# Performance work log

Measured on AMD Instinct MI355X. Metric: run time of the kernel, lower is better.

The kernel has to match this reference:

```python
import jax, jax.numpy as jnp
import numpy as np

P = 3; C = 64; IMG = 48; G = IMG // P
D = C * P * P          # 576 embedding dim == flatten dim
NH = 12; HD = D // NH  # 48 head dim
HID = 4 * D            # 2304
NL = 4; S = G * G      # 256 patches
NQ = 6
QN, QP = -8.0, 7.0     # 4-bit signed LSQ range
EPS = 1e-5


def lsq(w):
    # LSQ fake-quant of weights, step size from LSQ init formula, STE rounding
    alpha = 2.0 * jnp.mean(jnp.abs(w)) / jnp.sqrt(QP)
    q = jnp.clip(w / alpha, QN, QP)
    q = q + jax.lax.stop_gradient(jnp.round(q) - q)
    return q * alpha


def qlinear(x, w, b=None):
    y = x @ lsq(w).T
    return y if b is None else y + b


def ln(x, g, b):
    m = jnp.mean(x, -1, keepdims=True)
    v = jnp.var(x, -1, keepdims=True)
    return (x - m) / jnp.sqrt(v + EPS) * g + b


def mha(q, k, v, in_w, out_w):
    # q,k,v: [S,B,D]; in_w: [3D,D]; out_w: [D,D]; no biases
    Wq, Wk, Wv = jnp.split(lsq(in_w), 3, axis=0)
    def heads(t, W):
        return (t @ W.T).reshape(t.shape[0], t.shape[1], NH, HD)
    qh = heads(q, Wq) * (1.0 / jnp.sqrt(HD))
    kh = heads(k, Wk)
    vh = heads(v, Wv)
    att = jax.nn.softmax(jnp.einsum('qbhd,kbhd->bhqk', qh, kh), axis=-1)
    o = jnp.einsum('bhqk,kbhd->qbhd', att, vh).reshape(q.shape[0], q.shape[1], D)
    return o @ lsq(out_w).T


def _forward(x, lin_enc_w, lin_enc_b, pos_emb, query_embed_w,
             enc_in_w, enc_out_w, enc_l1_w, enc_l1_b, enc_l2_w, enc_l2_b,
             enc_ln1_g, enc_ln1_b, enc_ln2_g, enc_ln2_b,
             dec_sa_in_w, dec_sa_out_w, dec_ca_in_w, dec_ca_out_w,
             dec_l1_w, dec_l1_b, dec_l2_w, dec_l2_b,
             dec_ln1_g, dec_ln1_b, dec_ln2_g, dec_ln2_b, dec_ln3_g, dec_ln3_b,
             head1_w, head1_b, head2_w, head2_b, query_idx):
    B = x.shape[0]
    # unfold -> [S,B,flat], channel-major patch flattening like F.unfold
    t = x.reshape(B, C, G, P, G, P).transpose(0, 1, 3, 5, 2, 4)
    t = t.reshape(B, C * P * P, G * G).transpose(2, 0, 1)  # [S,B,D]
    t = qlinear(t, lin_enc_w, lin_enc_b) + t
    qe = query_embed_w[query_idx].reshape(S, 1, D)   # query_pos, broadcasts over B
    pos = pos_emb[:, None, :]                        # [S,1,D]
    h = t + pos
    for l in range(NL):  # encoder (pre-norm)
        h2 = ln(h, enc_ln1_g[l], enc_ln1_b[l])
        h = h + mha(h2, h2, h2, enc_in_w[l], enc_out_w[l])
        h2 = ln(h, enc_ln2_g[l], enc_ln2_b[l])
        h = h + qlinear(jax.nn.relu(qlinear(h2, enc_l1_w[l], enc_l1_b[l])), enc_l2_w[l], enc_l2_b[l])
    mem = h
    o = mem
    for l in range(NL):  # decoder, memory = encoder output
        o2 = ln(o, dec_ln1_g[l], dec_ln1_b[l])
        qk = o2 + qe
        o = o + mha(qk, qk, o2, dec_sa_in_w[l], dec_sa_out_w[l])
        o2 = ln(o, dec_ln2_g[l], dec_ln2_b[l])
        o = o + mha(o2 + qe, mem, mem, dec_ca_in_w[l], dec_ca_out_w[l])
        o2 = ln(o, dec_ln3_g[l], dec_ln3_b[l])
        o = o + qlinear(jax.nn.relu(qlinear(o2, dec_l1_w[l], dec_l1_b[l])), dec_l2_w[l], dec_l2_b[l])
    # mlp_head with residual
    o = o + qlinear(jax.nn.relu(qlinear(o, head1_w, head1_b)), head2_w, head2_b)
    # fold back: [S,B,D] -> [B,C,IMG,IMG]
    y = o.transpose(1, 2, 0).reshape(B, C, P, P, G, G).transpose(0, 1, 4, 2, 5, 3)
    return y.reshape(B, C, IMG, IMG)


def setup_inputs() -> dict:
    key = jax.random.key(0)
    ks = iter(jax.random.split(key, 64))
    def w(shape):
        return jax.random.normal(next(ks), shape, jnp.float32) * 0.02
    B = 4
    inp = {
        'x': jax.random.normal(next(ks), (B, C, IMG, IMG), jnp.float32),
        'lin_enc_w': w((D, D)), 'lin_enc_b': jnp.zeros((D,), jnp.float32),
        'pos_emb': w((S, D)),
        'query_embed_w': w((NQ, S * D)),
        'enc_in_w': w((NL, 3 * D, D)), 'enc_out_w': w((NL, D, D)),
        'enc_l1_w': w((NL, HID, D)), 'enc_l1_b': jnp.zeros((NL, HID), jnp.float32),
        'enc_l2_w': w((NL, D, HID)), 'enc_l2_b': jnp.zeros((NL, D), jnp.float32),
        'enc_ln1_g': jnp.ones((NL, D), jnp.float32), 'enc_ln1_b': jnp.zeros((NL, D), jnp.float32),
        'enc_ln2_g': jnp.ones((NL, D), jnp.float32), 'enc_ln2_b': jnp.zeros((NL, D), jnp.float32),
        'dec_sa_in_w': w((NL, 3 * D, D)), 'dec_sa_out_w': w((NL, D, D)),
        'dec_ca_in_w': w((NL, 3 * D, D)), 'dec_ca_out_w': w((NL, D, D)),
        'dec_l1_w': w((NL, HID, D)), 'dec_l1_b': jnp.zeros((NL, HID), jnp.float32),
        'dec_l2_w': w((NL, D, HID)), 'dec_l2_b': jnp.zeros((NL, D), jnp.float32),
        'dec_ln1_g': jnp.ones((NL, D), jnp.float32), 'dec_ln1_b': jnp.zeros((NL, D), jnp.float32),
        'dec_ln2_g': jnp.ones((NL, D), jnp.float32), 'dec_ln2_b': jnp.zeros((NL, D), jnp.float32),
        'dec_ln3_g': jnp.ones((NL, D), jnp.float32), 'dec_ln3_b': jnp.zeros((NL, D), jnp.float32),
        'head1_w': w((HID, D)), 'head1_b': jnp.zeros((HID,), jnp.float32),
        'head2_w': w((D, HID)), 'head2_b': jnp.zeros((D,), jnp.float32),
        'query_idx': 0,
    }
    return inp


def reference(x, lin_enc_w, lin_enc_b, pos_emb, query_embed_w,
              enc_in_w, enc_out_w, enc_l1_w, enc_l1_b, enc_l2_w, enc_l2_b,
              enc_ln1_g, enc_ln1_b, enc_ln2_g, enc_ln2_b,
              dec_sa_in_w, dec_sa_out_w, dec_ca_in_w, dec_ca_out_w,
              dec_l1_w, dec_l1_b, dec_l2_w, dec_l2_b,
              dec_ln1_g, dec_ln1_b, dec_ln2_g, dec_ln2_b, dec_ln3_g, dec_ln3_b,
              head1_w, head1_b, head2_w, head2_b, query_idx):
    return _forward(x, lin_enc_w, lin_enc_b, pos_emb, query_embed_w,
                    enc_in_w, enc_out_w, enc_l1_w, enc_l1_b, enc_l2_w, enc_l2_b,
                    enc_ln1_g, enc_ln1_b, enc_ln2_g, enc_ln2_b,
                    dec_sa_in_w, dec_sa_out_w, dec_ca_in_w, dec_ca_out_w,
                    dec_l1_w, dec_l1_b, dec_l2_w, dec_l2_b,
                    dec_ln1_g, dec_ln1_b, dec_ln2_g, dec_ln2_b, dec_ln3_g, dec_ln3_b,
                    head1_w, head1_b, head2_w, head2_b, query_idx)
```

## Files before the change

### kernel.cpp

```cpp
#include <hip/hip_runtime.h>
#include <cstddef>

#define Pp    3
#define Cc    64
#define IMGi  48
#define Gg    16
#define Dd    576
#define NHh   12
#define HDd   48
#define HIDh  2304
#define NLl   4
#define Ss    256
#define Bb    4
#define Mm    1024
#define EPSf  1e-5f
#define NJOBS 43
#define NSTAT 20

typedef short short8 __attribute__((ext_vector_type(8)));
typedef short short4v __attribute__((ext_vector_type(4)));
typedef float f32x4  __attribute__((ext_vector_type(4)));
typedef unsigned short ushort_t;

struct QJobs { const float* ptr[NJOBS]; int n[NJOBS]; int off[NJOBS]; };

__device__ __forceinline__ short f2bf(float f) {
  unsigned u = __float_as_uint(f);
  u = u + 0x7fffu + ((u >> 16) & 1u);
  return (short)(u >> 16);
}
__device__ __forceinline__ float bf2f(short s) {
  return __uint_as_float(((unsigned)(unsigned short)s) << 16);
}

typedef __attribute__((address_space(3))) unsigned lds_u32;
typedef __attribute__((address_space(1))) const unsigned glob_u32;
__device__ __forceinline__ void gload_lds16(const void* g, void* l) {
  __builtin_amdgcn_global_load_lds((glob_u32*)g, (lds_u32*)l, 16, 0, 0);
}


__global__ void k_zero(float* p, int n) {
  int i = blockIdx.x * blockDim.x + threadIdx.x;
  if (i < n) p[i] = 0.f;
}

__global__ void k_abssum(QJobs jobs, float* absum) {
  int job = blockIdx.x >> 7, blk = blockIdx.x & 127;
  const float4* p4 = (const float4*)jobs.ptr[job];
  int n4 = jobs.n[job] >> 2;
  float s0 = 0.f, s1 = 0.f, s2 = 0.f, s3 = 0.f;
  for (int i = blk * 1024 + threadIdx.x; i < n4; i += 128 * 1024) {
    float4 v = p4[i];
    s0 += fabsf(v.x) + fabsf(v.y) + fabsf(v.z) + fabsf(v.w);
    int i1 = i + 256;
    if (i1 < n4) { float4 w = p4[i1]; s1 += fabsf(w.x) + fabsf(w.y) + fabsf(w.z) + fabsf(w.w); }
    int i2 = i + 512;
    if (i2 < n4) { float4 w = p4[i2]; s2 += fabsf(w.x) + fabsf(w.y) + fabsf(w.z) + fabsf(w.w); }
    int i3 = i + 768;
    if (i3 < n4) { float4 w = p4[i3]; s3 += fabsf(w.x) + fabsf(w.y) + fabsf(w.z) + fabsf(w.w); }
  }
  float s = (s0 + s1) + (s2 + s3);
  #pragma unroll
  for (int o = 32; o; o >>= 1) s += __shfl_xor(s, o);
  __shared__ float red[4];
  if ((threadIdx.x & 63) == 0) red[threadIdx.x >> 6] = s;
  __syncthreads();
  if (threadIdx.x == 0) atomicAdd(&absum[job], (red[0] + red[1]) + (red[2] + red[3]));
}

__global__ void k_alpha(QJobs jobs, const float* absum, float* alpha, float* inva) {
  int j = threadIdx.x;
  if (j < NJOBS) {
    float a = 2.f * (absum[j] / (float)jobs.n[j]) / sqrtf(7.f);
    alpha[j] = a;
    inva[j] = 1.f / a;
  }
}

__device__ __forceinline__ short8 quant8(const float* p, float ia) {
  const float4* p4 = (const float4*)p;
  float4 w0 = p4[0], w1 = p4[1];
  short8 bv;
  bv[0] = f2bf(rintf(fminf(7.f, fmaxf(-8.f, w0.x * ia))));
  bv[1] = f2bf(rintf(fminf(7.f, fmaxf(-8.f, w0.y * ia))));
  bv[2] = f2bf(rintf(fminf(7.f, fmaxf(-8.f, w0.z * ia))));
  bv[3] = f2bf(rintf(fminf(7.f, fmaxf(-8.f, w0.w * ia))));
  bv[4] = f2bf(rintf(fminf(7.f, fmaxf(-8.f, w1.x * ia))));
  bv[5] = f2bf(rintf(fminf(7.f, fmaxf(-8.f, w1.y * ia))));
  bv[6] = f2bf(rintf(fminf(7.f, fmaxf(-8.f, w1.z * ia))));
  bv[7] = f2bf(rintf(fminf(7.f, fmaxf(-8.f, w1.w * ia))));
  return bv;
}

__global__ void k_quant(QJobs jobs, const float* __restrict__ inva, short* __restrict__ wq) {
  int job = blockIdx.x >> 7, blk = blockIdx.x & 127;
  const float* p = jobs.ptr[job];
  int n8 = jobs.n[job] >> 3;
  short* dst = wq + (size_t)jobs.off[job];
  float ia = inva[job];
  for (int i = blk * 1024 + threadIdx.x; i < n8; i += 128 * 1024) {
    *(short8*)(dst + (size_t)i * 8) = quant8(p + (size_t)i * 8, ia);
    int i1 = i + 256;
    if (i1 < n8) *(short8*)(dst + (size_t)i1 * 8) = quant8(p + (size_t)i1 * 8, ia);
    int i2 = i + 512;
    if (i2 < n8) *(short8*)(dst + (size_t)i2 * 8) = quant8(p + (size_t)i2 * 8, ia);
    int i3 = i + 768;
    if (i3 < n8) *(short8*)(dst + (size_t)i3 * 8) = quant8(p + (size_t)i3 * 8, ia);
  }
}

__global__ void k_patchify(const float* __restrict__ x, float* __restrict__ t,
                           ushort_t* __restrict__ tb) {
  int i = blockIdx.x * 256 + threadIdx.x;
  if (i >= Mm * Dd) return;
  int d = i % Dd, row = i / Dd;
  int b = row % Bb, s = row / Bb;
  int c = d / 9, r = d % 9;
  int p1 = r / 3, p2 = r % 3;
  int g1 = s / Gg, g2 = s % Gg;
  float v = x[((size_t)(b * Cc + c) * IMGi + (g1 * Pp + p1)) * IMGi + (g2 * Pp + p2)];
  t[i] = v;
  tb[i] = (ushort_t)f2bf(v);
}

__global__ void k_unpatch(const float* __restrict__ h, float* __restrict__ out) {
  int i = blockIdx.x * 256 + threadIdx.x;
  if (i >= Bb * Cc * IMGi * IMGi) return;
  int j = i % IMGi, t = i / IMGi;
  int r = t % IMGi; t /= IMGi;
  int c = t % Cc;
  int b = t / Cc;
  int g1 = r / Pp, p1 = r % Pp, g2 = j / Pp, p2 = j % Pp;
  int s = g1 * Gg + g2;
  int d = c * 9 + p1 * 3 + p2;
  out[i] = h[(size_t)(s * Bb + b) * Dd + d];
}

#define MT 64
#define NT 64
#define KC 288
#define LDKB 304
#define PANEL (NT * LDKB)
#define BCHUNKS 38

__device__ __forceinline__ int bswz(int row, int colByte) {
  return row * (LDKB * 2) + (colByte ^ (((row >> 2) & 3) << 4));
}

__device__ __forceinline__ void stage_async(const ushort_t* base, int ld,
                                            char* lds, int wave, int lane) {
  #pragma unroll
  for (int j = 0; j < 10; ++j) {
    const int c = wave * 10 + j;
    if (c < BCHUNKS) {
      const int p = c * 512 + lane * 8;
      const int prow = p / LDKB;
      const int pcol2 = (p % LDKB) * 2;
      const int lcol = pcol2 ^ (((prow >> 2) & 3) << 4);
      const ushort_t* src = (lcol < 576)
        ? base + (size_t)prow * ld + (lcol >> 1)
        : base;
      gload_lds16(src, lds + c * 1024);
    }
  }
}

template <int DB>
__global__ __launch_bounds__(256)
void k_gemm_mfma(const ushort_t* __restrict__ Xa, const ushort_t* __restrict__ Xb,
                 int n_split, int ldx,
                 const float* __restrict__ qe, const int* __restrict__ qidx,
                 const float* __restrict__ lng, const float* __restrict__ lnb,
                 const float* __restrict__ statA, const float* __restrict__ statB,
                 const float* __restrict__ Wraw, const short* __restrict__ Wq,
                 const float* __restrict__ bias, const float* __restrict__ pos,
                 const float* res, int ldr,
                 float* out, int ldo,
                 ushort_t* outbf, ushort_t* outbf2, float* statOut,
                 int N, int K,
                 const float* __restrict__ alpha_p, const float* __restrict__ inva_p,
                 int slot, int relu)
{
  __shared__ short As[DB * PANEL];
  __shared__ short Bs[DB * PANEL];
  const int tid  = threadIdx.x;
  const int wave = tid >> 6, lane = tid & 63;
  const int quad = lane >> 4, l15 = lane & 15;
  const int tile_m = blockIdx.y * MT, tile_n = blockIdx.x * NT;
  const int m_off = (wave >> 1) * 32, n_off = (wave & 1) * 32;
  const int sr = tid >> 2;
  const int sc = (tid & 3) * 8;
  const float inva = inva_p[slot];

  const bool isA = (!Xb || tile_n < n_split);
  const ushort_t* X = isA ? Xa : Xb;
  const bool addqe = (qe != nullptr) && isA;
  const float* stat = isA ? statA : statB;
  const bool a_reg = (stat != nullptr) || addqe;
  size_t qe_off = 0;
  if (addqe) qe_off = (size_t)qidx[0] * ((size_t)Ss * Dd);

  float mean = 0.f, sinv = 1.f;
  if (stat) {
    float2 st = *(const float2*)&stat[2 * (tile_m + sr)];
    mean = st.x * (1.f / (float)Dd);
    float var = st.y * (1.f / (float)Dd) - mean * mean;
    sinv = rsqrtf(var + EPSf);
  }

  f32x4 acc00 = {0,0,0,0}, acc01 = {0,0,0,0}, acc10 = {0,0,0,0}, acc11 = {0,0,0,0};

  auto STAGE = [&](int kc, int buf) {
    short* Asb = As + buf * PANEL;
    short* Bsb = Bs + buf * PANEL;
    if (Wq) {
      stage_async((const ushort_t*)Wq + (size_t)tile_n * K + kc, K,
                  (char*)Bsb, wave, lane);
    } else {
      const float* wr = Wraw + (size_t)(tile_n + sr) * K + kc;
      #pragma unroll
      for (int j = 0; j < 9; ++j) {
        const int k = sc + j * 32;
        short8 bv;
        bv = quant8(wr + k, inva);
        *(short8*)((char*)Bsb + bswz(sr, k * 2)) = bv;
      }
    }
    if (!a_reg) {
      stage_async(X + (size_t)tile_m * ldx + kc, ldx, (char*)Asb, wave, lane);
    } else {
      const int arow = tile_m + sr;
      const ushort_t* xr = X + (size_t)arow * ldx + kc;
      const float* qr = addqe ? (qe + qe_off + (size_t)(arow >> 2) * Dd + kc) : nullptr;
      #pragma unroll
      for (int j = 0; j < 9; ++j) {
        const int k = sc + j * 32;
        short8 xv = *(const short8*)(xr + k);
        float a[8];
        #pragma unroll
        for (int e = 0; e < 8; ++e) a[e] = bf2f(xv[e]);
        if (stat) {
          float4 g0 = *(const float4*)(lng + kc + k);
          float4 g1 = *(const float4*)(lng + kc + k + 4);
          float4 b0 = *(const float4*)(lnb + kc + k);
          float4 b1 = *(const float4*)(lnb + kc + k + 4);
          a[0] = (a[0] - mean) * sinv * g0.x + b0.x;
          a[1] = (a[1] - mean) * sinv * g0.y + b0.y;
          a[2] = (a[2] - mean) * sinv * g0.z + b0.z;
          a[3] = (a[3] - mean) * sinv * g0.w + b0.w;
          a[4] = (a[4] - mean) * sinv * g1.x + b1.x;
          a[5] = (a[5] - mean) * sinv * g1.y + b1.y;
          a[6] = (a[6] - mean) * sinv * g1.z + b1.z;
          a[7] = (a[7] - mean) * sinv * g1.w + b1.w;
        }
        if (addqe) {
          float4 q0 = *(const float4*)(qr + k);
          float4 q1 = *(const float4*)(qr + k + 4);
          a[0] += q0.x; a[1] += q0.y; a[2] += q0.z; a[3] += q0.w;
          a[4] += q1.x; a[5] += q1.y; a[6] += q1.z; a[7] += q1.w;
        }
        short8 av;
        #pragma unroll
        for (int e = 0; e < 8; ++e) av[e] = f2bf(a[e]);
        *(short8*)((char*)Asb + bswz(sr, k * 2)) = av;
      }
    }
  };

  auto COMPUTE = [&](int buf) {
    const short* Asb = As + buf * PANEL;
    const short* Bsb = Bs + buf * PANEL;
    #pragma unroll 3
    for (int ks = 0; ks < KC / 32; ++ks) {
      const int kb = ks * 32 + quad * 8;
      short8 af0 = *(const short8*)((const char*)Asb + bswz(m_off + l15, kb * 2));
      short8 af1 = *(const short8*)((const char*)Asb + bswz(m_off + 16 + l15, kb * 2));
      short8 bf0 = *(const short8*)((const char*)Bsb + bswz(n_off + l15, kb * 2));
      short8 bf1 = *(const short8*)((const char*)Bsb + bswz(n_off + 16 + l15, kb * 2));
      acc00 = __builtin_amdgcn_mfma_f32_16x16x32_bf16(af0, bf0, acc00, 0, 0, 0);
      acc01 = __builtin_amdgcn_mfma_f32_16x16x32_bf16(af0, bf1, acc01, 0, 0, 0);
      acc10 = __builtin_amdgcn_mfma_f32_16x16x32_bf16(af1, bf0, acc10, 0, 0, 0);
      acc11 = __builtin_amdgcn_mfma_f32_16x16x32_bf16(af1, bf1, acc11, 0, 0, 0);
    }
  };

  const int nc = K / KC;
  if (DB == 2) {
    STAGE(0, 0);
    __syncthreads();
    for (int c = 0; c < nc; ++c) {
      if (c + 1 < nc) STAGE((c + 1) * KC, (c + 1) & 1);
      COMPUTE(c & 1);
      __syncthreads();
    }
  } else {
    for (int c = 0; c < nc; ++c) {
      STAGE(c * KC, 0);
      __syncthreads();
      COMPUTE(0);
      __syncthreads();
    }
  }

  const float a_s = alpha_p[slot];
  const int rowb = tile_m + m_off + quad * 4;
  const int colb = tile_n + n_off + l15;
  f32x4 accs[4] = {acc00, acc01, acc10, acc11};
  float vsum[2][4], vsq[2][4];
  #pragma unroll
  for (int rt = 0; rt < 2; ++rt)
    #pragma unroll
    for (int r = 0; r < 4; ++r) { vsum[rt][r] = 0.f; vsq[rt][r] = 0.f; }

  #pragma unroll
  for (int t = 0; t < 4; ++t) {
    int row0 = rowb + ((t >> 1) * 16);
    int col  = colb + ((t & 1) * 16);
    float bv = bias ? bias[col] : 0.f;
    #pragma unroll
    for (int r = 0; r < 4; ++r) {
      int row = row0 + r;
      float v = accs[t][r] * a_s + bv;
      if (res) v += res[(size_t)row * ldr + col];
      if (pos) v += pos[(size_t)(row >> 2) * Dd + col];
      if (relu) v = fmaxf(v, 0.f);
      if (out)    out[(size_t)row * ldo + col] = v;
      if (outbf)  outbf[(size_t)row * ldo + col]  = (ushort_t)f2bf(v);
      if (outbf2) outbf2[(size_t)row * ldo + col] = (ushort_t)f2bf(v);
      vsum[t >> 1][r] += v;
      vsq[t >> 1][r]  += v * v;
    }
  }

  if (statOut) {
    #pragma unroll
    for (int rt = 0; rt < 2; ++rt) {
      #pragma unroll
      for (int r = 0; r < 4; ++r) {
        float s = vsum[rt][r], q = vsq[rt][r];
        #pragma unroll
        for (int o = 1; o < 16; o <<= 1) {
          s += __shfl_xor(s, o);
          q += __shfl_xor(q, o);
        }
        if (l15 == 0) {
          int row = rowb + rt * 16 + r;
          atomicAdd(&statOut[2 * row],     s);
          atomicAdd(&statOut[2 * row + 1], q);
        }
      }
    }
  }
}

__global__ __launch_bounds__(256)
void k_attn(const ushort_t* __restrict__ QKV, ushort_t* __restrict__ ctx, float scale) {
  __shared__ short Ks[256][72];
  __shared__ short Qs[64][72];
  __shared__ short Vt[48][264];
  __shared__ short Pq[64][264];
  const int qt = blockIdx.x;
  const int b  = blockIdx.y / NHh, h = blockIdx.y % NHh;
  const int tid = threadIdx.x;
  const int w = tid >> 6, lane = tid & 63, quad = lane >> 4, l15 = lane & 15;

  {
    const ushort_t* kp = QKV + (size_t)(tid * Bb + b) * 1728 + Dd + h * HDd;
    #pragma unroll
    for (int d0 = 0; d0 < 48; d0 += 8)
      *(short8*)&Ks[tid][d0] = *(const short8*)(kp + d0);
    short4v z = {0, 0, 0, 0};
    *(short4v*)&Ks[tid][48] = z; *(short4v*)&Ks[tid][52] = z;
    *(short4v*)&Ks[tid][56] = z; *(short4v*)&Ks[tid][60] = z;
    const ushort_t* vp = QKV + (size_t)(tid * Bb + b) * 1728 + 2 * Dd + h * HDd;
    #pragma unroll
    for (int d0 = 0; d0 < 48; d0 += 8) {
      short8 v = *(const short8*)(vp + d0);
      #pragma unroll
      for (int e = 0; e < 8; ++e) Vt[d0 + e][tid] = v[e];
    }
    if (tid < 64) {
      const ushort_t* qp = QKV + (size_t)((qt * 64 + tid) * Bb + b) * 1728 + h * HDd;
      #pragma unroll
      for (int d0 = 0; d0 < 48; d0 += 8)
        *(short8*)&Qs[tid][d0] = *(const short8*)(qp + d0);
      *(short4v*)&Qs[tid][48] = z; *(short4v*)&Qs[tid][52] = z;
      *(short4v*)&Qs[tid][56] = z; *(short4v*)&Qs[tid][60] = z;
    }
  }
  __syncthreads();

  short8 bq0 = *(short8*)&Qs[w * 16 + l15][quad * 8];
  short8 bq1 = *(short8*)&Qs[w * 16 + l15][32 + quad * 8];
  f32x4 sf[16];
  #pragma unroll
  for (int mt = 0; mt < 16; ++mt) {
    f32x4 acc = {0, 0, 0, 0};
    short8 a0 = *(short8*)&Ks[mt * 16 + l15][quad * 8];
    short8 a1 = *(short8*)&Ks[mt * 16 + l15][32 + quad * 8];
    acc = __builtin_amdgcn_mfma_f32_16x16x32_bf16(a0, bq0, acc, 0, 0, 0);
    acc = __builtin_amdgcn_mfma_f32_16x16x32_bf16(a1, bq1, acc, 0, 0, 0);
    sf[mt] = acc;
  }

  float mx = -1e30f;
  #pragma unroll
  for (int mt = 0; mt < 16; ++mt)
    #pragma unroll
    for (int r = 0; r < 4; ++r) {
      sf[mt][r] *= scale;
      mx = fmaxf(mx, sf[mt][r]);
    }
  mx = fmaxf(mx, __shfl_xor(mx, 16));
  mx = fmaxf(mx, __shfl_xor(mx, 32));
  float sum = 0.f;
  #pragma unroll
  for (int mt = 0; mt < 16; ++mt)
    #pragma unroll
    for (int r = 0; r < 4; ++r) {
      float e = __expf(sf[mt][r] - mx);
      sf[mt][r] = e;
      sum += e;
    }
  sum += __shfl_xor(sum, 16);
  sum += __shfl_xor(sum, 32);
  float inv = 1.f / sum;

  #pragma unroll
  for (int mt = 0; mt < 16; ++mt) {
    short4v p = { f2bf(sf[mt][0] * inv), f2bf(sf[mt][1] * inv),
                  f2bf(sf[mt][2] * inv), f2bf(sf[mt][3] * inv) };
    *(short4v*)&Pq[w * 16 + l15][mt * 16 + quad * 4] = p;
  }
  __syncthreads();

  f32x4 of0 = {0,0,0,0}, of1 = {0,0,0,0}, of2 = {0,0,0,0};
  #pragma unroll
  for (int kt = 0; kt < 8; ++kt) {
    short8 a = *(short8*)&Pq[w * 16 + l15][kt * 32 + quad * 8];
    short8 b0 = *(short8*)&Vt[l15][kt * 32 + quad * 8];
    short8 b1 = *(short8*)&Vt[16 + l15][kt * 32 + quad * 8];
    short8 b2 = *(short8*)&Vt[32 + l15][kt * 32 + quad * 8];
    of0 = __builtin_amdgcn_mfma_f32_16x16x32_bf16(a, b0, of0, 0, 0, 0);
    of1 = __builtin_amdgcn_mfma_f32_16x16x32_bf16(a, b1, of1, 0, 0, 0);
    of2 = __builtin_amdgcn_mfma_f32_16x16x32_bf16(a, b2, of2, 0, 0, 0);
  }
  const int qg = qt * 64 + w * 16 + quad * 4;
  #pragma unroll
  for (int r = 0; r < 4; ++r) {
    ushort_t* cr = ctx + (size_t)((qg + r) * Bb + b) * Dd + h * HDd + l15;
    cr[0]  = (ushort_t)f2bf(of0[r]);
    cr[16] = (ushort_t)f2bf(of1[r]);
    cr[32] = (ushort_t)f2bf(of2[r]);
  }
}


extern "C" void kernel_launch(void* const* d_in, const int* in_sizes, int n_in,
                              void* d_out, int out_size, void* d_ws, size_t ws_size,
                              hipStream_t stream) {
  (void)in_sizes; (void)n_in; (void)out_size;
  const float* x            = (const float*)d_in[0];
  const float* lin_enc_w    = (const float*)d_in[1];
  const float* lin_enc_b    = (const float*)d_in[2];
  const float* pos_emb      = (const float*)d_in[3];
  const float* query_embed  = (const float*)d_in[4];
  const float* enc_in_w     = (const float*)d_in[5];
  const float* enc_out_w    = (const float*)d_in[6];
  const float* enc_l1_w     = (const float*)d_in[7];
  const float* enc_l1_b     = (const float*)d_in[8];
  const float* enc_l2_w     = (const float*)d_in[9];
  const float* enc_l2_b     = (const float*)d_in[10];
  const float* enc_ln1_g    = (const float*)d_in[11];
  const float* enc_ln1_b    = (const float*)d_in[12];
  const float* enc_ln2_g    = (const float*)d_in[13];
  const float* enc_ln2_b    = (const float*)d_in[14];
  const float* dec_sa_in_w  = (const float*)d_in[15];
  const float* dec_sa_out_w = (const float*)d_in[16];
  const float* dec_ca_in_w  = (const float*)d_in[17];
  const float* dec_ca_out_w = (const float*)d_in[18];
  const float* dec_l1_w     = (const float*)d_in[19];
  const float* dec_l1_b     = (const float*)d_in[20];
  const float* dec_l2_w     = (const float*)d_in[21];
  const float* dec_l2_b     = (const float*)d_in[22];
  const float* dec_ln1_g    = (const float*)d_in[23];
  const float* dec_ln1_b    = (const float*)d_in[24];
  const float* dec_ln2_g    = (const float*)d_in[25];
  const float* dec_ln2_b    = (const float*)d_in[26];
  const float* dec_ln3_g    = (const float*)d_in[27];
  const float* dec_ln3_b    = (const float*)d_in[28];
  const float* head1_w      = (const float*)d_in[29];
  const float* head1_b      = (const float*)d_in[30];
  const float* head2_w      = (const float*)d_in[31];
  const float* head2_b      = (const float*)d_in[32];
  const int*   query_idx    = (const int*)d_in[33];
  float* out = (float*)d_out;

  const int DD  = Dd * Dd;
  const int IN3 = 3 * Dd * Dd;
  const int FF  = HIDh * Dd;
  const int MD  = Mm * Dd;

  float* ws = (float*)d_ws;
  float* ABSUM = ws;
  float* ALPHA = ws + 64;
  float* INVA  = ws + 128;
  float* STAT  = ws + 256;
  const int STATF = NSTAT * Mm * 2;
  float* H   = STAT + STATF;
  float* SCR = H + MD;
  ushort_t* Hb   = (ushort_t*)(SCR + MD);
  ushort_t* SCRb = Hb + MD;
  ushort_t* MEMb = SCRb + MD;
  ushort_t* CTXb = MEMb + MD;
  ushort_t* QKVb = CTXb + MD;
  size_t act_bytes = (256 + (size_t)STATF + 2 * (size_t)MD) * 4
                   + (4 * (size_t)MD + (size_t)Mm * HIDh) * 2;
  short* WQ = (short*)(QKVb + (size_t)Mm * HIDh);
  const size_t WQ_ELEMS = (size_t)DD + 4 * ((size_t)IN3 + DD + FF + FF)
                        + 4 * ((size_t)IN3 + DD + IN3 + DD + FF + FF)
                        + 2 * (size_t)FF;
  const bool use_wq = ws_size >= act_bytes + WQ_ELEMS * 2;

  auto T = [&](int i) { return STAT + (size_t)i * (Mm * 2); };

  QJobs jobs;
  int j = 0; int off = 0;
  auto addjob = [&](const float* p, int n) { jobs.ptr[j] = p; jobs.n[j] = n; jobs.off[j] = off; off += n; j++; };
  addjob(lin_enc_w, DD);
  for (int l = 0; l < NLl; ++l) addjob(enc_in_w  + (size_t)l * IN3, IN3);
  for (int l = 0; l < NLl; ++l) addjob(enc_out_w + (size_t)l * DD,  DD);
  for (int l = 0; l < NLl; ++l) addjob(enc_l1_w  + (size_t)l * FF,  FF);
  for (int l = 0; l < NLl; ++l) addjob(enc_l2_w  + (size_t)l * FF,  FF);
  for (int l = 0; l < NLl; ++l) addjob(dec_sa_in_w  + (size_t)l * IN3, IN3);
  for (int l = 0; l < NLl; ++l) addjob(dec_sa_out_w + (size_t)l * DD,  DD);
  for (int l = 0; l < NLl; ++l) addjob(dec_ca_in_w  + (size_t)l * IN3, IN3);
  for (int l = 0; l < NLl; ++l) addjob(dec_ca_out_w + (size_t)l * DD,  DD);
  for (int l = 0; l < NLl; ++l) addjob(dec_l1_w + (size_t)l * FF, FF);
  for (int l = 0; l < NLl; ++l) addjob(dec_l2_w + (size_t)l * FF, FF);
  addjob(head1_w, FF);
  addjob(head2_w, FF);

  const int ZN = 256 + STATF;
  k_zero<<<(ZN + 255) / 256, 256, 0, stream>>>(ws, ZN);
  k_abssum<<<NJOBS * 128, 256, 0, stream>>>(jobs, ABSUM);
  k_alpha<<<1, 64, 0, stream>>>(jobs, ABSUM, ALPHA, INVA);
  if (use_wq) k_quant<<<NJOBS * 128, 256, 0, stream>>>(jobs, INVA, WQ);

  auto gemm = [&](const ushort_t* Xa, const ushort_t* Xb, int n_split, int ldx,
                  const float* qe, const float* lng, const float* lnb,
                  const float* statA, const float* statB,
                  const float* W, int slot, const float* bias, const float* pos,
                  const float* res, int ldr,
                  float* o, int ldo, ushort_t* obf, ushort_t* obf2,
                  float* statOut, int N, int K, int relu) {
    dim3 grid(N / NT, Mm / MT);
    const short* wq = use_wq ? WQ + (size_t)jobs.off[slot] : nullptr;
    const float* wr = use_wq ? nullptr : W;
    if (K > 2 * KC)
      k_gemm_mfma<2><<<grid, 256, 0, stream>>>(Xa, Xb, n_split, ldx, qe, query_idx,
                                               lng, lnb, statA, statB,
                                               wr, wq, bias, pos, res, ldr,
                                               o, ldo, obf, obf2, statOut,
                                               N, K, ALPHA, INVA, slot, relu);
    else
      k_gemm_mfma<1><<<grid, 256, 0, stream>>>(Xa, Xb, n_split, ldx, qe, query_idx,
                                               lng, lnb, statA, statB,
                                               wr, wq, bias, pos, res, ldr,
                                               o, ldo, obf, obf2, statOut,
                                               N, K, ALPHA, INVA, slot, relu);
  };

  const float scale = 1.f / sqrtf((float)HDd);
  auto attn = [&](const float* out_w, int out_slot, float* statOut) {
    k_attn<<<dim3(Ss / 64, Bb * NHh), 256, 0, stream>>>(QKVb, CTXb, scale);
    gemm(CTXb, nullptr, 0, Dd, nullptr, nullptr, nullptr, nullptr, nullptr,
         out_w, out_slot, nullptr, nullptr, H, Dd,
         H, Dd, Hb, nullptr, statOut, Dd, Dd, 0);
  };

  const int NELEM = Mm * Dd;
  const int EB = (NELEM + 255) / 256;

  k_patchify<<<EB, 256, 0, stream>>>(x, SCR, SCRb);
  gemm(SCRb, nullptr, 0, Dd, nullptr, nullptr, nullptr, nullptr, nullptr,
       lin_enc_w, 0, lin_enc_b, pos_emb, SCR, Dd,
       H, Dd, Hb, nullptr, T(0), Dd, Dd, 0);

  for (int l = 0; l < NLl; ++l) {
    gemm(Hb, nullptr, 0, Dd, nullptr, enc_ln1_g + l * Dd, enc_ln1_b + l * Dd,
         T(2 * l), nullptr,
         enc_in_w + (size_t)l * IN3, 1 + l,
         nullptr, nullptr, nullptr, 0,
         nullptr, 1728, QKVb, nullptr, nullptr, 1728, Dd, 0);
    attn(enc_out_w + (size_t)l * DD, 5 + l, T(2 * l + 1));
    gemm(Hb, nullptr, 0, Dd, nullptr, enc_ln2_g + l * Dd, enc_ln2_b + l * Dd,
         T(2 * l + 1), nullptr,
         enc_l1_w + (size_t)l * FF, 9 + l,
         enc_l1_b + l * HIDh, nullptr, nullptr, 0,
         nullptr, HIDh, QKVb, nullptr, nullptr, HIDh, Dd, 1);
    gemm(QKVb, nullptr, 0, HIDh, nullptr, nullptr, nullptr, nullptr, nullptr,
         enc_l2_w + (size_t)l * FF, 13 + l,
         enc_l2_b + l * Dd, nullptr, H, Dd,
         H, Dd, Hb, (l == NLl - 1) ? MEMb : nullptr, T(2 * l + 2),
         Dd, HIDh, 0);
  }

  for (int l = 0; l < NLl; ++l) {
    float* ln1s = T(8 + 3 * l);
    gemm(Hb, Hb, 2 * Dd, Dd, query_embed,
         dec_ln1_g + l * Dd, dec_ln1_b + l * Dd, ln1s, ln1s,
         dec_sa_in_w + (size_t)l * IN3, 17 + l,
         nullptr, nullptr, nullptr, 0,
         nullptr, 1728, QKVb, nullptr, nullptr, 1728, Dd, 0);
    attn(dec_sa_out_w + (size_t)l * DD, 21 + l, T(9 + 3 * l));
    gemm(Hb, MEMb, Dd, Dd, query_embed,
         dec_ln2_g + l * Dd, dec_ln2_b + l * Dd, T(9 + 3 * l), nullptr,
         dec_ca_in_w + (size_t)l * IN3, 25 + l,
         nullptr, nullptr, nullptr, 0,
         nullptr, 1728, QKVb, nullptr, nullptr, 1728, Dd, 0);
    attn(dec_ca_out_w + (size_t)l * DD, 29 + l, T(10 + 3 * l));
    gemm(Hb, nullptr, 0, Dd, nullptr, dec_ln3_g + l * Dd, dec_ln3_b + l * Dd,
         T(10 + 3 * l), nullptr,
         dec_l1_w + (size_t)l * FF, 33 + l,
         dec_l1_b + l * HIDh, nullptr, nullptr, 0,
         nullptr, HIDh, QKVb, nullptr, nullptr, HIDh, Dd, 1);
    gemm(QKVb, nullptr, 0, HIDh, nullptr, nullptr, nullptr, nullptr, nullptr,
         dec_l2_w + (size_t)l * FF, 37 + l,
         dec_l2_b + l * Dd, nullptr, H, Dd,
         H, Dd, Hb, nullptr, (l < NLl - 1) ? T(11 + 3 * l) : nullptr,
         Dd, HIDh, 0);
  }

  gemm(Hb, nullptr, 0, Dd, nullptr, nullptr, nullptr, nullptr, nullptr,
       head1_w, 41, head1_b, nullptr, nullptr, 0,
       nullptr, HIDh, QKVb, nullptr, nullptr, HIDh, Dd, 1);
  gemm(QKVb, nullptr, 0, HIDh, nullptr, nullptr, nullptr, nullptr, nullptr,
       head2_w, 42, head2_b, nullptr, H, Dd,
       H, Dd, nullptr, nullptr, nullptr, Dd, HIDh, 0);

  k_unpatch<<<EB, 256, 0, stream>>>(H, out);
}
```

Measured before the change: 1.316 ms.

## Fuse unpatch into final GEMM, drop zero kernel, add XCD-aware tile remap

The final head2 GEMM epilogue now writes directly in image layout, which removes the separate unpatch kernel. The zeroing kernel and the float atomics in abssum are replaced by per-block partial sums that k_alpha reduces, and k_alpha also zeroes the stat buffer. GEMM workgroup ids are remapped so consecutive tiles land on the same XCD, which should improve L2 reuse. The scattered image-layout stores in the epilogue are uncoalesced, and k_alpha now does a serial 128-element reduction per job.

New measurement: 1.364 ms. 3.6% more time.

```diff
diff --git a/kernel.cpp b/kernel.cpp
--- a/kernel.cpp
+++ b/kernel.cpp
@@ -16,6 +16,7 @@
 #define EPSf  1e-5f
 #define NJOBS 43
 #define NSTAT 20
+#define ABLK  128
 
 typedef short short8 __attribute__((ext_vector_type(8)));
 typedef short short4v __attribute__((ext_vector_type(4)));
@@ -40,17 +41,12 @@
 }
 
 
-__global__ void k_zero(float* p, int n) {
-  int i = blockIdx.x * blockDim.x + threadIdx.x;
-  if (i < n) p[i] = 0.f;
-}
-
-__global__ void k_abssum(QJobs jobs, float* absum) {
+__global__ void k_abssum(QJobs jobs, float* absum2) {
   int job = blockIdx.x >> 7, blk = blockIdx.x & 127;
   const float4* p4 = (const float4*)jobs.ptr[job];
   int n4 = jobs.n[job] >> 2;
   float s0 = 0.f, s1 = 0.f, s2 = 0.f, s3 = 0.f;
-  for (int i = blk * 1024 + threadIdx.x; i < n4; i += 128 * 1024) {
+  for (int i = blk * 1024 + threadIdx.x; i < n4; i += ABLK * 1024) {
     float4 v = p4[i];
     s0 += fabsf(v.x) + fabsf(v.y) + fabsf(v.z) + fabsf(v.w);
     int i1 = i + 256;
@@ -66,16 +62,22 @@
   __shared__ float red[4];
   if ((threadIdx.x & 63) == 0) red[threadIdx.x >> 6] = s;
   __syncthreads();
-  if (threadIdx.x == 0) atomicAdd(&absum[job], (red[0] + red[1]) + (red[2] + red[3]));
-}
-
-__global__ void k_alpha(QJobs jobs, const float* absum, float* alpha, float* inva) {
-  int j = threadIdx.x;
-  if (j < NJOBS) {
-    float a = 2.f * (absum[j] / (float)jobs.n[j]) / sqrtf(7.f);
-    alpha[j] = a;
-    inva[j] = 1.f / a;
-  }
+  if (threadIdx.x == 0)
+    absum2[job * ABLK + blk] = (red[0] + red[1]) + (red[2] + red[3]);
+}
+
+__global__ void k_alpha(QJobs jobs, const float* __restrict__ absum2,
+                        float* alpha, float* inva, float* stat, int statn) {
+  int t = threadIdx.x;
+  if (t < NJOBS) {
+    float s = 0.f;
+    const float* p = absum2 + t * ABLK;
+    for (int i = 0; i < ABLK; ++i) s += p[i];
+    float a = 2.f * (s / (float)jobs.n[t]) / sqrtf(7.f);
+    alpha[t] = a;
+    inva[t] = 1.f / a;
+  }
+  for (int i = t; i < statn; i += 256) stat[i] = 0.f;
 }
 
 __device__ __forceinline__ short8 quant8(const float* p, float ia) {
@@ -124,19 +126,6 @@
   tb[i] = (ushort_t)f2bf(v);
 }
 
-__global__ void k_unpatch(const float* __restrict__ h, float* __restrict__ out) {
-  int i = blockIdx.x * 256 + threadIdx.x;
-  if (i >= Bb * Cc * IMGi * IMGi) return;
-  int j = i % IMGi, t = i / IMGi;
-  int r = t % IMGi; t /= IMGi;
-  int c = t % Cc;
-  int b = t / Cc;
-  int g1 = r / Pp, p1 = r % Pp, g2 = j / Pp, p2 = j % Pp;
-  int s = g1 * Gg + g2;
-  int d = c * 9 + p1 * 3 + p2;
-  out[i] = h[(size_t)(s * Bb + b) * Dd + d];
-}
-
 #define MT 64
 #define NT 64
 #define KC 288
@@ -180,14 +169,26 @@
                  ushort_t* outbf, ushort_t* outbf2, float* statOut,
                  int N, int K,
                  const float* __restrict__ alpha_p, const float* __restrict__ inva_p,
-                 int slot, int relu)
+                 int slot, int relu, int unpat)
 {
   __shared__ short As[DB * PANEL];
   __shared__ short Bs[DB * PANEL];
   const int tid  = threadIdx.x;
   const int wave = tid >> 6, lane = tid & 63;
   const int quad = lane >> 4, l15 = lane & 15;
-  const int tile_m = blockIdx.y * MT, tile_n = blockIdx.x * NT;
+
+  const int gx = gridDim.x, gy = gridDim.y;
+  const int nwg = gx * gy;
+  const int id = blockIdx.x + gx * blockIdx.y;
+  const int q = nwg >> 3, rr = nwg & 7;
+  const int xcd = id & 7, o = id >> 3;
+  const int tile = (xcd < rr) ? (xcd * (q + 1) + o)
+                              : (rr * (q + 1) + (xcd - rr) * q + o);
+  int tn_i, tm_i;
+  if (N >= Mm) { tn_i = tile / gy; tm_i = tile % gy; }
+  else         { tm_i = tile / gx; tn_i = tile % gx; }
+  const int tile_m = tm_i * MT, tile_n = tn_i * NT;
+
   const int m_off = (wave >> 1) * 32, n_off = (wave & 1) * 32;
   const int sr = tid >> 2;
   const int sc = (tid & 3) * 8;
@@ -222,9 +223,7 @@
       #pragma unroll
       for (int j = 0; j < 9; ++j) {
         const int k = sc + j * 32;
-        short8 bv;
-        bv = quant8(wr + k, inva);
-        *(short8*)((char*)Bsb + bswz(sr, k * 2)) = bv;
+        *(short8*)((char*)Bsb + bswz(sr, k * 2)) = quant8(wr + k, inva);
       }
     }
     if (!a_reg) {
@@ -325,7 +324,15 @@
       if (res) v += res[(size_t)row * ldr + col];
       if (pos) v += pos[(size_t)(row >> 2) * Dd + col];
       if (relu) v = fmaxf(v, 0.f);
-      if (out)    out[(size_t)row * ldo + col] = v;
+      if (unpat) {
+        int b = row & 3, s = row >> 2;
+        int c = col / 9, rm = col % 9;
+        int p1 = rm / 3, p2 = rm % 3;
+        int g1 = s >> 4, g2 = s & 15;
+        out[((size_t)(b * Cc + c) * IMGi + g1 * 3 + p1) * IMGi + (g2 * 3 + p2)] = v;
+      } else if (out) {
+        out[(size_t)row * ldo + col] = v;
+      }
       if (outbf)  outbf[(size_t)row * ldo + col]  = (ushort_t)f2bf(v);
       if (outbf2) outbf2[(size_t)row * ldo + col] = (ushort_t)f2bf(v);
       vsum[t >> 1][r] += v;
@@ -338,16 +345,16 @@
     for (int rt = 0; rt < 2; ++rt) {
       #pragma unroll
       for (int r = 0; r < 4; ++r) {
-        float s = vsum[rt][r], q = vsq[rt][r];
+        float s = vsum[rt][r], qv = vsq[rt][r];
         #pragma unroll
-        for (int o = 1; o < 16; o <<= 1) {
-          s += __shfl_xor(s, o);
-          q += __shfl_xor(q, o);
+        for (int o2 = 1; o2 < 16; o2 <<= 1) {
+          s  += __shfl_xor(s, o2);
+          qv += __shfl_xor(qv, o2);
         }
         if (l15 == 0) {
           int row = rowb + rt * 16 + r;
           atomicAdd(&statOut[2 * row],     s);
-          atomicAdd(&statOut[2 * row + 1], q);
+          atomicAdd(&statOut[2 * row + 1], qv);
         }
       }
     }
@@ -503,10 +510,10 @@
   const int MD  = Mm * Dd;
 
   float* ws = (float*)d_ws;
-  float* ABSUM = ws;
-  float* ALPHA = ws + 64;
-  float* INVA  = ws + 128;
-  float* STAT  = ws + 256;
+  float* ABSUM2 = ws;
+  float* ALPHA  = ws + 5632;
+  float* INVA   = ws + 5696;
+  float* STAT   = ws + 5760;
   const int STATF = NSTAT * Mm * 2;
   float* H   = STAT + STATF;
   float* SCR = H + MD;
@@ -515,9 +522,9 @@
   ushort_t* MEMb = SCRb + MD;
   ushort_t* CTXb = MEMb + MD;
   ushort_t* QKVb = CTXb + MD;
-  size_t act_bytes = (256 + (size_t)STATF + 2 * (size_t)MD) * 4
+  short* WQ = (short*)(QKVb + (size_t)Mm * HIDh);
+  size_t act_bytes = (5760 + (size_t)STATF + 2 * (size_t)MD) * 4
                    + (4 * (size_t)MD + (size_t)Mm * HIDh) * 2;
-  short* WQ = (short*)(QKVb + (size_t)Mm * HIDh);
   const size_t WQ_ELEMS = (size_t)DD + 4 * ((size_t)IN3 + DD + FF + FF)
                         + 4 * ((size_t)IN3 + DD + IN3 + DD + FF + FF)
                         + 2 * (size_t)FF;
@@ -542,10 +549,8 @@
   addjob(head1_w, FF);
   addjob(head2_w, FF);
 
-  const int ZN = 256 + STATF;
-  k_zero<<<(ZN + 255) / 256, 256, 0, stream>>>(ws, ZN);
-  k_abssum<<<NJOBS * 128, 256, 0, stream>>>(jobs, ABSUM);
-  k_alpha<<<1, 64, 0, stream>>>(jobs, ABSUM, ALPHA, INVA);
+  k_abssum<<<NJOBS * ABLK, 256, 0, stream>>>(jobs, ABSUM2);
+  k_alpha<<<1, 256, 0, stream>>>(jobs, ABSUM2, ALPHA, INVA, STAT, STATF);
   if (use_wq) k_quant<<<NJOBS * 128, 256, 0, stream>>>(jobs, INVA, WQ);
 
   auto gemm = [&](const ushort_t* Xa, const ushort_t* Xb, int n_split, int ldx,
@@ -554,7 +559,7 @@
                   const float* W, int slot, const float* bias, const float* pos,
                   const float* res, int ldr,
                   float* o, int ldo, ushort_t* obf, ushort_t* obf2,
-                  float* statOut, int N, int K, int relu) {
+                  float* statOut, int N, int K, int relu, int unpat) {
     dim3 grid(N / NT, Mm / MT);
     const short* wq = use_wq ? WQ + (size_t)jobs.off[slot] : nullptr;
     const float* wr = use_wq ? nullptr : W;
@@ -563,13 +568,13 @@
                                                lng, lnb, statA, statB,
                                                wr, wq, bias, pos, res, ldr,
                                                o, ldo, obf, obf2, statOut,
-                                               N, K, ALPHA, INVA, slot, relu);
+                                               N, K, ALPHA, INVA, slot, relu, unpat);
     else
       k_gemm_mfma<1><<<grid, 256, 0, stream>>>(Xa, Xb, n_split, ldx, qe, query_idx,
                                                lng, lnb, statA, statB,
                                                wr, wq, bias, pos, res, ldr,
                                                o, ldo, obf, obf2, statOut,
-                                               N, K, ALPHA, INVA, slot, relu);
+                                               N, K, ALPHA, INVA, slot, relu, unpat);
   };
 
   const float scale = 1.f / sqrtf((float)HDd);
@@ -577,7 +582,7 @@
     k_attn<<<dim3(Ss / 64, Bb * NHh), 256, 0, stream>>>(QKVb, CTXb, scale);
     gemm(CTXb, nullptr, 0, Dd, nullptr, nullptr, nullptr, nullptr, nullptr,
          out_w, out_slot, nullptr, nullptr, H, Dd,
-         H, Dd, Hb, nullptr, statOut, Dd, Dd, 0);
+         H, Dd, Hb, nullptr, statOut, Dd, Dd, 0, 0);
   };
 
   const int NELEM = Mm * Dd;
@@ -586,25 +591,25 @@
   k_patchify<<<EB, 256, 0, stream>>>(x, SCR, SCRb);
   gemm(SCRb, nullptr, 0, Dd, nullptr, nullptr, nullptr, nullptr, nullptr,
        lin_enc_w, 0, lin_enc_b, pos_emb, SCR, Dd,
-       H, Dd, Hb, nullptr, T(0), Dd, Dd, 0);
+       H, Dd, Hb, nullptr, T(0), Dd, Dd, 0, 0);
 
   for (int l = 0; l < NLl; ++l) {
     gemm(Hb, nullptr, 0, Dd, nullptr, enc_ln1_g + l * Dd, enc_ln1_b + l * Dd,
          T(2 * l), nullptr,
          enc_in_w + (size_t)l * IN3, 1 + l,
          nullptr, nullptr, nullptr, 0,
-         nullptr, 1728, QKVb, nullptr, nullptr, 1728, Dd, 0);
+         nullptr, 1728, QKVb, nullptr, nullptr, 1728, Dd, 0, 0);
     attn(enc_out_w + (size_t)l * DD, 5 + l, T(2 * l + 1));
     gemm(Hb, nullptr, 0, Dd, nullptr, enc_ln2_g + l * Dd, enc_ln2_b + l * Dd,
          T(2 * l + 1), nullptr,
          enc_l1_w + (size_t)l * FF, 9 + l,
          enc_l1_b + l * HIDh, nullptr, nullptr, 0,
-         nullptr, HIDh, QKVb, nullptr, nullptr, HIDh, Dd, 1);
+         nullptr, HIDh, QKVb, nullptr, nullptr, HIDh, Dd, 1, 0);
     gemm(QKVb, nullptr, 0, HIDh, nullptr, nullptr, nullptr, nullptr, nullptr,
          enc_l2_w + (size_t)l * FF, 13 + l,
          enc_l2_b + l * Dd, nullptr, H, Dd,
          H, Dd, Hb, (l == NLl - 1) ? MEMb : nullptr, T(2 * l + 2),
-         Dd, HIDh, 0);
+         Dd, HIDh, 0, 0);
   }
 
   for (int l = 0; l < NLl; ++l) {
@@ -613,32 +618,30 @@
          dec_ln1_g + l * Dd, dec_ln1_b + l * Dd, ln1s, ln1s,
          dec_sa_in_w + (size_t)l * IN3, 17 + l,
          nullptr, nullptr, nullptr, 0,
-         nullptr, 1728, QKVb, nullptr, nullptr, 1728, Dd, 0);
+         nullptr, 1728, QKVb, nullptr, nullptr, 1728, Dd, 0, 0);
     attn(dec_sa_out_w + (size_t)l * DD, 21 + l, T(9 + 3 * l));
     gemm(Hb, MEMb, Dd, Dd, query_embed,
          dec_ln2_g + l * Dd, dec_ln2_b + l * Dd, T(9 + 3 * l), nullptr,
          dec_ca_in_w + (size_t)l * IN3, 25 + l,
          nullptr, nullptr, nullptr, 0,
-         nullptr, 1728, QKVb, nullptr, nullptr, 1728, Dd, 0);
+         nullptr, 1728, QKVb, nullptr, nullptr, 1728, Dd, 0, 0);
     attn(dec_ca_out_w + (size_t)l * DD, 29 + l, T(10 + 3 * l));
     gemm(Hb, nullptr, 0, Dd, nullptr, dec_ln3_g + l * Dd, dec_ln3_b + l * Dd,
          T(10 + 3 * l), nullptr,
          dec_l1_w + (size_t)l * FF, 33 + l,
          dec_l1_b + l * HIDh, nullptr, nullptr, 0,
-         nullptr, HIDh, QKVb, nullptr, nullptr, HIDh, Dd, 1);
+         nullptr, HIDh, QKVb, nullptr, nullptr, HIDh, Dd, 1, 0);
     gemm(QKVb, nullptr, 0, HIDh, nullptr, nullptr, nullptr, nullptr, nullptr,
          dec_l2_w + (size_t)l * FF, 37 + l,
          dec_l2_b + l * Dd, nullptr, H, Dd,
          H, Dd, Hb, nullptr, (l < NLl - 1) ? T(11 + 3 * l) : nullptr,
-         Dd, HIDh, 0);
+         Dd, HIDh, 0, 0);
   }
 
   gemm(Hb, nullptr, 0, Dd, nullptr, nullptr, nullptr, nullptr, nullptr,
        head1_w, 41, head1_b, nullptr, nullptr, 0,
-       nullptr, HIDh, QKVb, nullptr, nullptr, HIDh, Dd, 1);
+       nullptr, HIDh, QKVb, nullptr, nullptr, HIDh, Dd, 1, 0);
   gemm(QKVb, nullptr, 0, HIDh, nullptr, nullptr, nullptr, nullptr, nullptr,
        head2_w, 42, head2_b, nullptr, H, Dd,
-       H, Dd, nullptr, nullptr, nullptr, Dd, HIDh, 0);
-
-  k_unpatch<<<EB, 256, 0, stream>>>(H, out);
-}
+       out, Dd, nullptr, nullptr, nullptr, Dd, HIDh, 0, 1);
+}
```
